# Kernel tuning notes

Hardware: AMD Instinct MI355X
Metric: run time of the kernel (lower is better)

Reference implementation:

```python
import jax, jax.numpy as jnp
import numpy as np

B, S, D = 8, 1024, 768
H, HD = 12, 64  # heads, head dim (H*HD == D)
EPS = 1e-12


def setup_inputs() -> dict:
    key = jax.random.key(0)
    ks = jax.random.split(key, 8)
    s = 0.02
    return {
        "hidden_states": jax.random.normal(ks[0], (B, S, D), jnp.float32),
        "attention_mask": jnp.zeros((B, 1, 1, S), jnp.float32),
        "head_mask": jnp.ones((H,), jnp.float32),
        "Wq": jax.random.normal(ks[1], (D, H * HD), jnp.float32) * s,
        "bq": jnp.zeros((H * HD,), jnp.float32),
        "Wk": jax.random.normal(ks[2], (D, H * HD), jnp.float32) * s,
        "bk": jnp.zeros((H * HD,), jnp.float32),
        "Wv": jax.random.normal(ks[3], (D, H * HD), jnp.float32) * s,
        "bv": jnp.zeros((H * HD,), jnp.float32),
        "Wo": jax.random.normal(ks[4], (D, H * HD), jnp.float32) * s,  # torch Linear weight [out=D, in=H*HD]
        "bo": jnp.zeros((D,), jnp.float32),
        "gamma": jnp.ones((D,), jnp.float32),
        "beta": jnp.zeros((D,), jnp.float32),
    }


def reference(hidden_states, attention_mask, head_mask, Wq, bq, Wk, bk, Wv, bv, Wo, bo, gamma, beta):
    def heads(x):  # [B,S,H*HD] -> [B,H,S,HD]
        return x.reshape(B, S, H, HD).transpose(0, 2, 1, 3)

    q = heads(hidden_states @ Wq.T + bq)
    k = heads(hidden_states @ Wk.T + bk)
    v = heads(hidden_states @ Wv.T + bv)

    scores = jnp.einsum("bhqd,bhkd->bhqk", q, k) / np.sqrt(HD).astype(np.float32)
    scores = scores + attention_mask
    probs = jax.nn.softmax(scores, axis=-1)  # dropout p=0 (eval)
    ctx = jnp.einsum("bhqk,bhkd->bhqd", probs, v)  # [B,H,S,HD]

    # masked per-head output projection: Wo.T.view(H, HD, D)
    Wph = Wo.T.reshape(H, HD, D)
    proj = jnp.einsum("bhsd,hde,h->bse", ctx, Wph, head_mask) + bo

    # residual + LayerNorm
    x = proj + hidden_states
    mu = jnp.mean(x, axis=-1, keepdims=True)
    var = jnp.mean(jnp.square(x - mu), axis=-1, keepdims=True)
    out = (x - mu) * jax.lax.rsqrt(var + EPS) * gamma + beta
    return out
```

## Files before the change

kernel.cpp:

```cpp
#include <hip/hip_runtime.h>
#include <hip/hip_bf16.h>
#include <math.h>

#define Bn 8
#define Sn 1024
#define Dn 768
#define Hn 12
#define MROWS (Bn * Sn)

typedef __attribute__((ext_vector_type(8))) short short8;
typedef __attribute__((ext_vector_type(4))) float floatx4;

__device__ __forceinline__ unsigned short f2b(float x) {
    union { float f; unsigned u; } v; v.f = x;
    unsigned r = v.u + 0x7fffu + ((v.u >> 16) & 1u);
    return (unsigned short)(r >> 16);
}

__device__ __forceinline__ unsigned pk2(float a, float b) {
    union { __hip_bfloat162 h; unsigned u; } v;
    v.h = __float22bfloat162_rn(float2{a, b});
    return v.u;
}

__device__ __forceinline__ float fexp2(float x) {
    float r;
    asm("v_exp_f32 %0, %1" : "=v"(r) : "v"(x));
    return r;
}

__device__ __forceinline__ void gload16(const void* g, void* l) {
    __builtin_amdgcn_global_load_lds(
        (const __attribute__((address_space(1))) void*)g,
        (__attribute__((address_space(3))) void*)l, 16, 0, 0);
}

#define MEMFENCE() asm volatile("" ::: "memory")
#define WAITV8()  asm volatile("s_waitcnt vmcnt(8)" ::: "memory")
#define WAITV6()  asm volatile("s_waitcnt vmcnt(6)" ::: "memory")
#define WAITV0()  asm volatile("s_waitcnt vmcnt(0)" ::: "memory")
#define WAITLGKM() asm volatile("s_waitcnt lgkmcnt(0)" ::: "memory")

__global__ __launch_bounds__(256) void convert_all(const float* __restrict__ X,
                                                   const float* __restrict__ Wq, const float* __restrict__ Wk,
                                                   const float* __restrict__ Wv, const float* __restrict__ Wo,
                                                   unsigned short* __restrict__ Xb,
                                                   unsigned short* __restrict__ Wqb, unsigned short* __restrict__ Wkb,
                                                   unsigned short* __restrict__ Wvb, unsigned short* __restrict__ Wob) {
    const int id = blockIdx.x;
    const float* src;
    unsigned short* dst;
    int i;
    if (id < 6144) {
        src = X; dst = Xb;
        i = id * 256 + threadIdx.x;
    } else {
        const int y = (id - 6144) / 576;
        src = (y == 0) ? Wq : (y == 1) ? Wk : (y == 2) ? Wv : Wo;
        dst = (y == 0) ? Wqb : (y == 1) ? Wkb : (y == 2) ? Wvb : Wob;
        i = ((id - 6144) % 576) * 256 + threadIdx.x;
    }
    float4 v = reinterpret_cast<const float4*>(src)[i];
    ushort4 o;
    o.x = f2b(v.x); o.y = f2b(v.y); o.z = f2b(v.z); o.w = f2b(v.w);
    reinterpret_cast<ushort4*>(dst)[i] = o;
}

#define QKV_COMPUTE(Ab, Wb)                                                    \
    {                                                                          \
        short8 af[4][2], bf[4][2];                                             \
        _Pragma("unroll") for (int i = 0; i < 4; i++)                          \
            _Pragma("unroll") for (int ks = 0; ks < 2; ks++) {                 \
                af[i][ks] = *(const short8*)&(Ab)[aoff[i][ks]];                \
                bf[i][ks] = *(const short8*)&(Wb)[woff[i][ks]];                \
            }                                                                  \
        __builtin_amdgcn_s_setprio(1);                                         \
        _Pragma("unroll") for (int ks = 0; ks < 2; ks++)                       \
            _Pragma("unroll") for (int i = 0; i < 4; i++)                      \
                _Pragma("unroll") for (int j = 0; j < 4; j++)                  \
                    acc[i][j] = __builtin_amdgcn_mfma_f32_16x16x32_bf16(       \
                        af[i][ks], bf[j][ks], acc[i][j], 0, 0, 0);             \
        __builtin_amdgcn_s_setprio(0);                                         \
    }

__global__ __launch_bounds__(256) void gemm_qkv(const unsigned short* __restrict__ A,
                                                const unsigned short* __restrict__ Wq,
                                                const unsigned short* __restrict__ Wk,
                                                const unsigned short* __restrict__ Wv,
                                                const float* __restrict__ bq,
                                                const float* __restrict__ bk,
                                                const float* __restrict__ bv,
                                                unsigned short* __restrict__ Qh,
                                                unsigned short* __restrict__ Kh,
                                                unsigned short* __restrict__ Vt) {
    __shared__ __align__(16) unsigned short As[2][128 * 64];
    __shared__ __align__(16) unsigned short Ws[2][128 * 64];
    const int id = blockIdx.x;
    const int by = id & 63;
    const int bx = id >> 6;
    const int mat = bx / 6;
    const int m0 = by * 128;
    const int n0 = (bx % 6) * 128;
    const unsigned short* W = (mat == 0) ? Wq : (mat == 1) ? Wk : Wv;
    const float* bias = (mat == 0) ? bq : (mat == 1) ? bk : bv;
    unsigned short* Cout = (mat == 0) ? Qh : (mat == 1) ? Kh : Vt;

    const int tid = threadIdx.x;
    const int w = tid >> 6, l = tid & 63, quad = l >> 4, mr = l & 15;
    const int wm = (w >> 1) * 64, wn = (w & 1) * 64;

    const unsigned short* gAsrc[4];
    const unsigned short* gWsrc[4];
    unsigned short* lAdst[4];
    unsigned short* lWdst[4];
#pragma unroll
    for (int j = 0; j < 4; j++) {
        const int u = tid + j * 256;
        const int r = u >> 3, c = u & 7;
        const int kq = (c ^ (r & 7)) * 8;
        gAsrc[j] = &A[(size_t)(m0 + r) * Dn + kq];
        gWsrc[j] = &W[(size_t)(n0 + r) * Dn + kq];
        lAdst[j] = &As[0][u * 8];
        lWdst[j] = &Ws[0][u * 8];
    }

    int aoff[4][2], woff[4][2];
#pragma unroll
    for (int i = 0; i < 4; i++) {
        const int ra = wm + i * 16 + mr;
        const int rw = wn + i * 16 + mr;
#pragma unroll
        for (int ks = 0; ks < 2; ks++) {
            aoff[i][ks] = (ra * 8 + ((quad + ks * 4) ^ (ra & 7))) * 8;
            woff[i][ks] = (rw * 8 + ((quad + ks * 4) ^ (rw & 7))) * 8;
        }
    }

    floatx4 acc[4][4];
#pragma unroll
    for (int i = 0; i < 4; i++)
#pragma unroll
        for (int j = 0; j < 4; j++) {
            floatx4 z = {0.f, 0.f, 0.f, 0.f};
            acc[i][j] = z;
        }

    const unsigned short* Af = &As[0][0];
    const unsigned short* Wf = &Ws[0][0];

#pragma unroll
    for (int j = 0; j < 4; j++) {
        gload16(gAsrc[j], lAdst[j]);
        gload16(gWsrc[j], lWdst[j]);
    }

    for (int kt = 0; kt < 12; kt += 2) {
        {
            const int k0 = (kt + 1) * 64;
#pragma unroll
            for (int j = 0; j < 4; j++) {
                gload16(gAsrc[j] + k0, lAdst[j] + 8192);
                gload16(gWsrc[j] + k0, lWdst[j] + 8192);
            }
        }
        WAITV8();
        __builtin_amdgcn_s_barrier();
        MEMFENCE();
        QKV_COMPUTE(Af, Wf);
        __builtin_amdgcn_s_barrier();
        MEMFENCE();

        if (kt + 2 < 12) {
            const int k0 = (kt + 2) * 64;
#pragma unroll
            for (int j = 0; j < 4; j++) {
                gload16(gAsrc[j] + k0, lAdst[j]);
                gload16(gWsrc[j] + k0, lWdst[j]);
            }
            WAITV8();
        } else {
            WAITV0();
        }
        __builtin_amdgcn_s_barrier();
        MEMFENCE();
        QKV_COMPUTE(Af + 8192, Wf + 8192);
        __builtin_amdgcn_s_barrier();
        MEMFENCE();
    }

#pragma unroll
    for (int j = 0; j < 4; j++) {
        const int col = n0 + wn + j * 16 + mr;
        const float bval = bias[col];
        const int h = col >> 6, d = col & 63;
#pragma unroll
        for (int i = 0; i < 4; i++) {
            const int mbase = m0 + wm + i * 16 + quad * 4;
            const int b = mbase >> 10, s0 = mbase & 1023;
            const size_t base = (size_t)(b * Hn + h) << 16;
            if (mat == 2) {
                ushort4 o;
                o.x = f2b(acc[i][j][0] + bval);
                o.y = f2b(acc[i][j][1] + bval);
                o.z = f2b(acc[i][j][2] + bval);
                o.w = f2b(acc[i][j][3] + bval);
                *reinterpret_cast<ushort4*>(&Cout[base + (size_t)d * 1024 + s0]) = o;
            } else {
#pragma unroll
                for (int r = 0; r < 4; r++) {
                    const float val = acc[i][j][r] + bval;
                    Cout[base + (size_t)(s0 + r) * 64 + d] = f2b(val);
                }
            }
        }
    }
}

#define OUT_COMPUTE(Ab, Wb)                                                    \
    {                                                                          \
        short8 af[4][2], bf[2][2];                                             \
        _Pragma("unroll") for (int i = 0; i < 4; i++)                          \
            _Pragma("unroll") for (int ks = 0; ks < 2; ks++)                   \
                af[i][ks] = *(const short8*)&(Ab)[aoff[i][ks]];                \
        _Pragma("unroll") for (int j = 0; j < 2; j++)                          \
            _Pragma("unroll") for (int ks = 0; ks < 2; ks++)                   \
                bf[j][ks] = *(const short8*)&(Wb)[woff[j][ks]];                \
        __builtin_amdgcn_s_setprio(1);                                         \
        _Pragma("unroll") for (int ks = 0; ks < 2; ks++)                       \
            _Pragma("unroll") for (int i = 0; i < 4; i++)                      \
                _Pragma("unroll") for (int j = 0; j < 2; j++)                  \
                    acc[i][j] = __builtin_amdgcn_mfma_f32_16x16x32_bf16(       \
                        af[i][ks], bf[j][ks], acc[i][j], 0, 0, 0);             \
        __builtin_amdgcn_s_setprio(0);                                         \
    }

__global__ __launch_bounds__(256) void gemm_out(const unsigned short* __restrict__ A,
                                                const unsigned short* __restrict__ W,
                                                const float* __restrict__ bias,
                                                const float* __restrict__ X,
                                                float* __restrict__ xres) {
    __shared__ __align__(16) unsigned short As[2][64 * 64];
    __shared__ __align__(16) unsigned short Ws[2][128 * 64];
    const int id = blockIdx.x;
    const int by = id & 127;
    const int bx = id >> 7;
    const int m0 = by * 64;
    const int n0 = bx * 128;

    const int tid = threadIdx.x;
    const int w = tid >> 6, l = tid & 63, quad = l >> 4, mr = l & 15;

    const unsigned short* gAsrc[2];
    unsigned short* lAdst[2];
#pragma unroll
    for (int j = 0; j < 2; j++) {
        const int u = tid + j * 256;
        const int r = u >> 3, c = u & 7;
        gAsrc[j] = &A[(size_t)(m0 + r) * Dn + (c ^ (r & 7)) * 8];
        lAdst[j] = &As[0][u * 8];
    }
    const unsigned short* gWsrc[4];
    unsigned short* lWdst[4];
#pragma unroll
    for (int j = 0; j < 4; j++) {
        const int u = tid + j * 256;
        const int r = u >> 3, c = u & 7;
        gWsrc[j] = &W[(size_t)(n0 + r) * Dn + (c ^ (r & 7)) * 8];
        lWdst[j] = &Ws[0][u * 8];
    }

    int aoff[4][2], woff[2][2];
#pragma unroll
    for (int i = 0; i < 4; i++) {
        const int ra = i * 16 + mr;
#pragma unroll
        for (int ks = 0; ks < 2; ks++)
            aoff[i][ks] = (ra * 8 + ((quad + ks * 4) ^ (ra & 7))) * 8;
    }
#pragma unroll
    for (int j = 0; j < 2; j++) {
        const int rw = w * 32 + j * 16 + mr;
#pragma unroll
        for (int ks = 0; ks < 2; ks++)
            woff[j][ks] = (rw * 8 + ((quad + ks * 4) ^ (rw & 7))) * 8;
    }

    floatx4 acc[4][2];
#pragma unroll
    for (int i = 0; i < 4; i++)
#pragma unroll
        for (int j = 0; j < 2; j++) {
            floatx4 z = {0.f, 0.f, 0.f, 0.f};
            acc[i][j] = z;
        }

    const unsigned short* Af = &As[0][0];
    const unsigned short* Wf = &Ws[0][0];

#pragma unroll
    for (int j = 0; j < 2; j++) gload16(gAsrc[j], lAdst[j]);
#pragma unroll
    for (int j = 0; j < 4; j++) gload16(gWsrc[j], lWdst[j]);

    for (int kt = 0; kt < 12; kt += 2) {
        {
            const int k0 = (kt + 1) * 64;
#pragma unroll
            for (int j = 0; j < 2; j++) gload16(gAsrc[j] + k0, lAdst[j] + 4096);
#pragma unroll
            for (int j = 0; j < 4; j++) gload16(gWsrc[j] + k0, lWdst[j] + 8192);
        }
        WAITV6();
        __builtin_amdgcn_s_barrier();
        MEMFENCE();
        OUT_COMPUTE(Af, Wf);
        __builtin_amdgcn_s_barrier();
        MEMFENCE();

        if (kt + 2 < 12) {
            const int k0 = (kt + 2) * 64;
#pragma unroll
            for (int j = 0; j < 2; j++) gload16(gAsrc[j] + k0, lAdst[j]);
#pragma unroll
            for (int j = 0; j < 4; j++) gload16(gWsrc[j] + k0, lWdst[j]);
            WAITV6();
        } else {
            WAITV0();
        }
        __builtin_amdgcn_s_barrier();
        MEMFENCE();
        OUT_COMPUTE(Af + 4096, Wf + 8192);
        __builtin_amdgcn_s_barrier();
        MEMFENCE();
    }

#pragma unroll
    for (int j = 0; j < 2; j++) {
        const int col = n0 + w * 32 + j * 16 + mr;
        const float bval = bias[col];
#pragma unroll
        for (int i = 0; i < 4; i++) {
#pragma unroll
            for (int r = 0; r < 4; r++) {
                const int m = m0 + i * 16 + quad * 4 + r;
                xres[(size_t)m * Dn + col] = acc[i][j][r] + bval + X[(size_t)m * Dn + col];
            }
        }
    }
}

__global__ __launch_bounds__(256) void flash_attn_mfma(const unsigned short* __restrict__ Qh,
                                                       const unsigned short* __restrict__ Kh,
                                                       const unsigned short* __restrict__ Vt,
                                                       const float* __restrict__ mask,
                                                       const float* __restrict__ head_mask,
                                                       unsigned short* __restrict__ ctx) {
    __shared__ __align__(16) unsigned short Ks[64 * 72];
    __shared__ __align__(16) unsigned short Vs[64 * 72];
    __shared__ __align__(16) unsigned short Ps[128 * 72];
    __shared__ float msk[64];

    const float LOG2E = 1.44269504088896f;
    const float C1 = 0.125f * 1.44269504088896f;

    const int id = blockIdx.x;
    const int bh = id % 96;
    const int qt = id / 96;
    const int b = bh / Hn, h = bh % Hn;
    const int q0 = qt * 128;
    const int tid = threadIdx.x;
    const int w = tid >> 6, l = tid & 63, quad = l >> 4, mr = l & 15;
    const size_t hb = (size_t)(b * Hn + h) << 16;

    short8 aq[2][2];
#pragma unroll
    for (int j = 0; j < 2; j++)
#pragma unroll
        for (int ks = 0; ks < 2; ks++)
            aq[j][ks] = *(const short8*)&Qh[hb + (size_t)(q0 + w * 32 + j * 16 + mr) * 64 + ks * 32 + quad * 8];

    float l_s[2] = {0.f, 0.f};
    floatx4 oacc[2][4];
#pragma unroll
    for (int i = 0; i < 2; i++)
#pragma unroll
        for (int jj = 0; jj < 4; jj++) {
            floatx4 z = {0.f, 0.f, 0.f, 0.f};
            oacc[i][jj] = z;
        }

    const int srow = tid >> 2;
    const int scol = (tid & 3) * 16;

    short8 pk0 = *(const short8*)&Kh[hb + (size_t)srow * 64 + scol];
    short8 pk1 = *(const short8*)&Kh[hb + (size_t)srow * 64 + scol + 8];
    short8 pv0 = *(const short8*)&Vt[hb + (size_t)srow * 1024 + scol];
    short8 pv1 = *(const short8*)&Vt[hb + (size_t)srow * 1024 + scol + 8];
    float pm = mask[b * Sn + (tid & 63)];

    for (int kt = 0; kt < Sn / 64; kt++) {
        __builtin_amdgcn_s_barrier();
        MEMFENCE();
        *(short8*)&Ks[srow * 72 + scol] = pk0;
        *(short8*)&Ks[srow * 72 + scol + 8] = pk1;
        *(short8*)&Vs[srow * 72 + scol] = pv0;
        *(short8*)&Vs[srow * 72 + scol + 8] = pv1;
        if (tid < 64) msk[tid] = pm * LOG2E;
        if (kt < Sn / 64 - 1) {
            const int k0 = (kt + 1) * 64;
            pk0 = *(const short8*)&Kh[hb + (size_t)(k0 + srow) * 64 + scol];
            pk1 = *(const short8*)&Kh[hb + (size_t)(k0 + srow) * 64 + scol + 8];
            pv0 = *(const short8*)&Vt[hb + (size_t)srow * 1024 + k0 + scol];
            pv1 = *(const short8*)&Vt[hb + (size_t)srow * 1024 + k0 + scol + 8];
            pm = mask[b * Sn + k0 + (tid & 63)];
        }
        WAITLGKM();
        __builtin_amdgcn_s_barrier();
        MEMFENCE();

        floatx4 sacc[4][2];
#pragma unroll
        for (int i = 0; i < 4; i++)
#pragma unroll
            for (int j = 0; j < 2; j++) {
                floatx4 z = {0.f, 0.f, 0.f, 0.f};
                sacc[i][j] = z;
            }
#pragma unroll
        for (int ks = 0; ks < 2; ks++) {
            short8 kfr[4];
#pragma unroll
            for (int i = 0; i < 4; i++)
                kfr[i] = *(const short8*)&Ks[(i * 16 + mr) * 72 + ks * 32 + quad * 8];
            __builtin_amdgcn_s_setprio(1);
#pragma unroll
            for (int i = 0; i < 4; i++)
#pragma unroll
                for (int j = 0; j < 2; j++)
                    sacc[i][j] = __builtin_amdgcn_mfma_f32_16x16x32_bf16(kfr[i], aq[j][ks], sacc[i][j], 0, 0, 0);
            __builtin_amdgcn_s_setprio(0);
        }

#pragma unroll
        for (int i = 0; i < 4; i++) {
            floatx4 mk4 = *(const floatx4*)&msk[i * 16 + quad * 4];
#pragma unroll
            for (int j = 0; j < 2; j++) {
                float p[4];
#pragma unroll
                for (int r = 0; r < 4; r++) {
                    p[r] = fexp2(sacc[i][j][r] * C1 + mk4[r]);
                    l_s[j] += p[r];
                }
                uint2 w2;
                w2.x = pk2(p[0], p[1]);
                w2.y = pk2(p[2], p[3]);
                *(uint2*)&Ps[(w * 32 + j * 16 + mr) * 72 + i * 16 + quad * 4] = w2;
            }
        }

#pragma unroll
        for (int ks = 0; ks < 2; ks++) {
            short8 ap0 = *(const short8*)&Ps[(w * 32 + mr) * 72 + ks * 32 + quad * 8];
            short8 ap1 = *(const short8*)&Ps[(w * 32 + 16 + mr) * 72 + ks * 32 + quad * 8];
            __builtin_amdgcn_s_setprio(1);
#pragma unroll
            for (int jj = 0; jj < 4; jj++) {
                short8 bv = *(const short8*)&Vs[(jj * 16 + mr) * 72 + ks * 32 + quad * 8];
                oacc[0][jj] = __builtin_amdgcn_mfma_f32_16x16x32_bf16(ap0, bv, oacc[0][jj], 0, 0, 0);
                oacc[1][jj] = __builtin_amdgcn_mfma_f32_16x16x32_bf16(ap1, bv, oacc[1][jj], 0, 0, 0);
            }
            __builtin_amdgcn_s_setprio(0);
        }
    }

    float L[2];
#pragma unroll
    for (int j = 0; j < 2; j++) {
        float t = l_s[j];
        t += __shfl_xor(t, 16);
        t += __shfl_xor(t, 32);
        L[j] = t;
    }
    const float hm = head_mask[h];
    float inv[2][4];
#pragma unroll
    for (int i = 0; i < 2; i++)
#pragma unroll
        for (int r = 0; r < 4; r++)
            inv[i][r] = hm / __shfl(L[i], quad * 4 + r);

#pragma unroll
    for (int i = 0; i < 2; i++)
#pragma unroll
        for (int jj = 0; jj < 4; jj++)
#pragma unroll
            for (int r = 0; r < 4; r++) {
                const int qrow = q0 + w * 32 + i * 16 + quad * 4 + r;
                ctx[(size_t)(b * Sn + qrow) * Dn + h * 64 + jj * 16 + mr] = f2b(oacc[i][jj][r] * inv[i][r]);
            }
}

__global__ __launch_bounds__(256) void ln_kernel(const float* __restrict__ x,
                                                 const float* __restrict__ gamma,
                                                 const float* __restrict__ beta,
                                                 float* __restrict__ out) {
    __shared__ float r1[4];
    __shared__ float r2[4];
    const int m = blockIdx.x;
    const int tid = threadIdx.x;
    const int w = tid >> 6, lane = tid & 63;

    float xv[3];
    float s = 0.f, ss = 0.f;
#pragma unroll
    for (int i = 0; i < 3; i++) {
        int j = tid + i * 256;
        float t = x[(size_t)m * Dn + j];
        xv[i] = t;
        s += t;
        ss += t * t;
    }
#pragma unroll
    for (int o = 1; o < 64; o <<= 1) {
        s += __shfl_xor(s, o);
        ss += __shfl_xor(ss, o);
    }
    if (lane == 0) { r1[w] = s; r2[w] = ss; }
    __syncthreads();
    const float sum = r1[0] + r1[1] + r1[2] + r1[3];
    const float sqs = r2[0] + r2[1] + r2[2] + r2[3];
    const float mu = sum * (1.0f / Dn);
    const float var = sqs * (1.0f / Dn) - mu * mu;
    const float rstd = rsqrtf(var + 1e-12f);
#pragma unroll
    for (int i = 0; i < 3; i++) {
        int j = tid + i * 256;
        out[(size_t)m * Dn + j] = (xv[i] - mu) * rstd * gamma[j] + beta[j];
    }
}

extern "C" void kernel_launch(void* const* d_in, const int* in_sizes, int n_in,
                              void* d_out, int out_size, void* d_ws, size_t ws_size,
                              hipStream_t stream) {
    const float* X         = (const float*)d_in[0];
    const float* mask      = (const float*)d_in[1];
    const float* head_mask = (const float*)d_in[2];
    const float* Wq        = (const float*)d_in[3];
    const float* bq        = (const float*)d_in[4];
    const float* Wk        = (const float*)d_in[5];
    const float* bk        = (const float*)d_in[6];
    const float* Wv        = (const float*)d_in[7];
    const float* bv        = (const float*)d_in[8];
    const float* Wo        = (const float*)d_in[9];
    const float* bo        = (const float*)d_in[10];
    const float* gamma     = (const float*)d_in[11];
    const float* beta      = (const float*)d_in[12];
    float* out = (float*)d_out;

    const size_t NE = (size_t)Bn * Sn * Dn;
    const size_t NW = (size_t)Dn * Dn;

    char* p = (char*)d_ws;
    unsigned short* Xb  = (unsigned short*)p;  p += NE * 2;
    unsigned short* Wqb = (unsigned short*)p;  p += NW * 2;
    unsigned short* Wkb = (unsigned short*)p;  p += NW * 2;
    unsigned short* Wvb = (unsigned short*)p;  p += NW * 2;
    unsigned short* Wob = (unsigned short*)p;  p += NW * 2;
    unsigned short* Qh  = (unsigned short*)p;  p += NE * 2;
    unsigned short* Kh  = (unsigned short*)p;  p += NE * 2;
    unsigned short* Vtb = (unsigned short*)p;  p += NE * 2;
    unsigned short* ctx = (unsigned short*)p;  p += NE * 2;
    float* xres = (float*)p;

    convert_all<<<8448, 256, 0, stream>>>(X, Wq, Wk, Wv, Wo, Xb, Wqb, Wkb, Wvb, Wob);

    gemm_qkv<<<1152, 256, 0, stream>>>(Xb, Wqb, Wkb, Wvb, bq, bk, bv, Qh, Kh, Vtb);

    flash_attn_mfma<<<768, 256, 0, stream>>>(Qh, Kh, Vtb, mask, head_mask, ctx);

    gemm_out<<<768, 256, 0, stream>>>(ctx, Wob, bo, X, xres);

    ln_kernel<<<MROWS, 256, 0, stream>>>(xres, gamma, beta, out);
}
```

Before: 213.2 us.

## Restructure QKV GEMM into triple-buffered K=32 pipeline with single barrier per stage

Changes the QKV projection GEMM from a double-buffered K=64 loop with two barriers per tile to a three-stage ring of K=32 tiles, issuing the next async global-to-LDS load right after a single barrier. LDS footprint per block drops from 64KB to 48KB and the launch bound asks for 3 blocks per CU, aiming for more occupancy and better overlap of loads with MFMA. The cost is more, smaller stages with more waits and barriers per unit of K work, plus a new swizzle layout that has to stay conflict-free.

```diff
diff --git a/kernel.cpp b/kernel.cpp
--- a/kernel.cpp
+++ b/kernel.cpp
@@ -38,6 +38,7 @@
 #define MEMFENCE() asm volatile("" ::: "memory")
 #define WAITV8()  asm volatile("s_waitcnt vmcnt(8)" ::: "memory")
 #define WAITV6()  asm volatile("s_waitcnt vmcnt(6)" ::: "memory")
+#define WAITV4()  asm volatile("s_waitcnt vmcnt(4)" ::: "memory")
 #define WAITV0()  asm volatile("s_waitcnt vmcnt(0)" ::: "memory")
 #define WAITLGKM() asm volatile("s_waitcnt lgkmcnt(0)" ::: "memory")
 
@@ -66,35 +67,44 @@
     reinterpret_cast<ushort4*>(dst)[i] = o;
 }
 
-#define QKV_COMPUTE(Ab, Wb)                                                    \
+#define QKV_STAGE(t, b)                                                        \
     {                                                                          \
-        short8 af[4][2], bf[4][2];                                             \
-        _Pragma("unroll") for (int i = 0; i < 4; i++)                          \
-            _Pragma("unroll") for (int ks = 0; ks < 2; ks++) {                 \
-                af[i][ks] = *(const short8*)&(Ab)[aoff[i][ks]];                \
-                bf[i][ks] = *(const short8*)&(Wb)[woff[i][ks]];                \
-            }                                                                  \
+        const int k0 = (t) * 32;                                               \
+        gload16(gAsrc[0] + k0, lAdst[0] + (b) * 4096);                         \
+        gload16(gAsrc[1] + k0, lAdst[1] + (b) * 4096);                         \
+        gload16(gWsrc[0] + k0, lWdst[0] + (b) * 4096);                         \
+        gload16(gWsrc[1] + k0, lWdst[1] + (b) * 4096);                         \
+    }
+
+#define QKV_COMP(b)                                                            \
+    {                                                                          \
+        const unsigned short* Ab = &As[b][0];                                  \
+        const unsigned short* Wb = &Ws[b][0];                                  \
+        short8 bf[4];                                                          \
+        _Pragma("unroll") for (int j = 0; j < 4; j++)                          \
+            bf[j] = *(const short8*)&Wb[woff[j]];                              \
         __builtin_amdgcn_s_setprio(1);                                         \
-        _Pragma("unroll") for (int ks = 0; ks < 2; ks++)                       \
-            _Pragma("unroll") for (int i = 0; i < 4; i++)                      \
-                _Pragma("unroll") for (int j = 0; j < 4; j++)                  \
-                    acc[i][j] = __builtin_amdgcn_mfma_f32_16x16x32_bf16(       \
-                        af[i][ks], bf[j][ks], acc[i][j], 0, 0, 0);             \
+        _Pragma("unroll") for (int i = 0; i < 4; i++) {                        \
+            short8 af = *(const short8*)&Ab[aoff[i]];                          \
+            _Pragma("unroll") for (int j = 0; j < 4; j++)                      \
+                acc[i][j] = __builtin_amdgcn_mfma_f32_16x16x32_bf16(           \
+                    af, bf[j], acc[i][j], 0, 0, 0);                            \
+        }                                                                      \
         __builtin_amdgcn_s_setprio(0);                                         \
     }
 
-__global__ __launch_bounds__(256) void gemm_qkv(const unsigned short* __restrict__ A,
-                                                const unsigned short* __restrict__ Wq,
-                                                const unsigned short* __restrict__ Wk,
-                                                const unsigned short* __restrict__ Wv,
-                                                const float* __restrict__ bq,
-                                                const float* __restrict__ bk,
-                                                const float* __restrict__ bv,
-                                                unsigned short* __restrict__ Qh,
-                                                unsigned short* __restrict__ Kh,
-                                                unsigned short* __restrict__ Vt) {
-    __shared__ __align__(16) unsigned short As[2][128 * 64];
-    __shared__ __align__(16) unsigned short Ws[2][128 * 64];
+__global__ __launch_bounds__(256, 3) void gemm_qkv(const unsigned short* __restrict__ A,
+                                                   const unsigned short* __restrict__ Wq,
+                                                   const unsigned short* __restrict__ Wk,
+                                                   const unsigned short* __restrict__ Wv,
+                                                   const float* __restrict__ bq,
+                                                   const float* __restrict__ bk,
+                                                   const float* __restrict__ bv,
+                                                   unsigned short* __restrict__ Qh,
+                                                   unsigned short* __restrict__ Kh,
+                                                   unsigned short* __restrict__ Vt) {
+    __shared__ __align__(16) unsigned short As[3][128 * 32];
+    __shared__ __align__(16) unsigned short Ws[3][128 * 32];
     const int id = blockIdx.x;
     const int by = id & 63;
     const int bx = id >> 6;
@@ -109,31 +119,31 @@
     const int w = tid >> 6, l = tid & 63, quad = l >> 4, mr = l & 15;
     const int wm = (w >> 1) * 64, wn = (w & 1) * 64;
 
-    const unsigned short* gAsrc[4];
-    const unsigned short* gWsrc[4];
-    unsigned short* lAdst[4];
-    unsigned short* lWdst[4];
-#pragma unroll
-    for (int j = 0; j < 4; j++) {
+    const unsigned short* gAsrc[2];
+    const unsigned short* gWsrc[2];
+    unsigned short* lAdst[2];
+    unsigned short* lWdst[2];
+#pragma unroll
+    for (int j = 0; j < 2; j++) {
         const int u = tid + j * 256;
-        const int r = u >> 3, c = u & 7;
-        const int kq = (c ^ (r & 7)) * 8;
-        gAsrc[j] = &A[(size_t)(m0 + r) * Dn + kq];
-        gWsrc[j] = &W[(size_t)(n0 + r) * Dn + kq];
+        const int r = u >> 2, c = u & 3;
+        const int cp = c ^ ((r >> 1) & 3);
+        gAsrc[j] = &A[(size_t)(m0 + r) * Dn + cp * 8];
+        gWsrc[j] = &W[(size_t)(n0 + r) * Dn + cp * 8];
         lAdst[j] = &As[0][u * 8];
         lWdst[j] = &Ws[0][u * 8];
     }
 
-    int aoff[4][2], woff[4][2];
+    int aoff[4], woff[4];
 #pragma unroll
     for (int i = 0; i < 4; i++) {
         const int ra = wm + i * 16 + mr;
-        const int rw = wn + i * 16 + mr;
-#pragma unroll
-        for (int ks = 0; ks < 2; ks++) {
-            aoff[i][ks] = (ra * 8 + ((quad + ks * 4) ^ (ra & 7))) * 8;
-            woff[i][ks] = (rw * 8 + ((quad + ks * 4) ^ (rw & 7))) * 8;
-        }
+        aoff[i] = (ra * 4 + (quad ^ ((ra >> 1) & 3))) * 8;
+    }
+#pragma unroll
+    for (int j = 0; j < 4; j++) {
+        const int rw = wn + j * 16 + mr;
+        woff[j] = (rw * 4 + (quad ^ ((rw >> 1) & 3))) * 8;
     }
 
     floatx4 acc[4][4];
@@ -145,48 +155,43 @@
             acc[i][j] = z;
         }
 
-    const unsigned short* Af = &As[0][0];
-    const unsigned short* Wf = &Ws[0][0];
-
-#pragma unroll
-    for (int j = 0; j < 4; j++) {
-        gload16(gAsrc[j], lAdst[j]);
-        gload16(gWsrc[j], lWdst[j]);
-    }
-
-    for (int kt = 0; kt < 12; kt += 2) {
-        {
-            const int k0 = (kt + 1) * 64;
-#pragma unroll
-            for (int j = 0; j < 4; j++) {
-                gload16(gAsrc[j] + k0, lAdst[j] + 8192);
-                gload16(gWsrc[j] + k0, lWdst[j] + 8192);
-            }
-        }
-        WAITV8();
-        __builtin_amdgcn_s_barrier();
-        MEMFENCE();
-        QKV_COMPUTE(Af, Wf);
-        __builtin_amdgcn_s_barrier();
-        MEMFENCE();
-
-        if (kt + 2 < 12) {
-            const int k0 = (kt + 2) * 64;
-#pragma unroll
-            for (int j = 0; j < 4; j++) {
-                gload16(gAsrc[j] + k0, lAdst[j]);
-                gload16(gWsrc[j] + k0, lWdst[j]);
-            }
-            WAITV8();
-        } else {
-            WAITV0();
-        }
-        __builtin_amdgcn_s_barrier();
-        MEMFENCE();
-        QKV_COMPUTE(Af + 8192, Wf + 8192);
-        __builtin_amdgcn_s_barrier();
-        MEMFENCE();
-    }
+    QKV_STAGE(0, 0);
+    QKV_STAGE(1, 1);
+
+    for (int t = 0; t < 21; t += 3) {
+        WAITV4();
+        __builtin_amdgcn_s_barrier();
+        MEMFENCE();
+        QKV_STAGE(t + 2, 2);
+        QKV_COMP(0);
+
+        WAITV4();
+        __builtin_amdgcn_s_barrier();
+        MEMFENCE();
+        QKV_STAGE(t + 3, 0);
+        QKV_COMP(1);
+
+        WAITV4();
+        __builtin_amdgcn_s_barrier();
+        MEMFENCE();
+        QKV_STAGE(t + 4, 1);
+        QKV_COMP(2);
+    }
+    WAITV4();
+    __builtin_amdgcn_s_barrier();
+    MEMFENCE();
+    QKV_STAGE(23, 2);
+    QKV_COMP(0);
+
+    WAITV4();
+    __builtin_amdgcn_s_barrier();
+    MEMFENCE();
+    QKV_COMP(1);
+
+    WAITV0();
+    __builtin_amdgcn_s_barrier();
+    MEMFENCE();
+    QKV_COMP(2);
 
 #pragma unroll
     for (int j = 0; j < 4; j++) {
```

After: 212.3 us. No clear change (-0.4%).
